# Kernel tuning notes

Hardware: AMD Instinct MI355X
Metric: run time of the kernel (lower is better)

Reference implementation:

```python
import jax, jax.numpy as jnp
import numpy as np

NEG_INF = -1e30


def setup_inputs() -> dict:
    key = jax.random.key(0)
    kq, kk, kv, ks = jax.random.split(key, 4)
    B, H, S, D = 2, 16, 2048, 64
    return {
        "q": jax.random.normal(kq, (B, H, S, D), dtype=jnp.float32),
        "k": jax.random.normal(kk, (B, H, S, D), dtype=jnp.float32),
        "v": jax.random.normal(kv, (B, H, S, D), dtype=jnp.float32),
        "sink_weights": jax.random.normal(ks, (H,), dtype=jnp.float32),
        "sliding_window": 1024,
    }


def reference(q, k, v, sink_weights, sliding_window):
    """Sliding-window causal attention with a learnable attention-sink logit.

    Equivalent to FlexAttention.forward with sink_weights given: an extra kv
    position (the sink) is appended whose score is replaced by sink_weights[h]
    and whose value is zero -> it only adds mass to the softmax denominator.
    """
    B, H, S_q, D = q.shape
    S_kv = k.shape[2]
    scale = 1.0 / np.sqrt(D)

    # [B, H, S_q, S_kv] raw scores
    scores = jnp.einsum("bhqd,bhkd->bhqk", q, k) * scale

    q_idx = jnp.arange(S_q)[:, None]
    kv_idx = jnp.arange(S_kv)[None, :]
    keep = (kv_idx <= q_idx) & (q_idx - kv_idx <= sliding_window)  # [S_q, S_kv]
    scores = jnp.where(keep[None, None], scores, NEG_INF)

    # sink column: per-head learnable logit, always visible
    sink_col = jnp.broadcast_to(
        sink_weights[None, :, None, None], (B, H, S_q, 1)
    )
    logits = jnp.concatenate([scores, sink_col], axis=-1)  # [B,H,S_q,S_kv+1]

    probs = jax.nn.softmax(logits, axis=-1)
    # sink value is zero, so only the first S_kv prob columns hit v
    out = jnp.einsum("bhqk,bhkd->bhqd", probs[..., :S_kv], v)
    return out
```

## Files before the change

kernel.cpp:

```cpp
#include <hip/hip_runtime.h>


typedef __bf16 bf16x8 __attribute__((ext_vector_type(8)));
typedef __bf16 bf16x4 __attribute__((ext_vector_type(4)));
typedef float  f32x16 __attribute__((ext_vector_type(16)));

#define NT 256
#define NEG_BIG (-3.0e38f)

__device__ __forceinline__ int swz(int row, int gran) {
    return row * 64 + ((gran ^ ((row >> 1) & 7)) << 3);
}

__device__ __forceinline__ bf16x4 xswap32(bf16x4 v) {
    union { bf16x4 v; int i[2]; } u;
    u.v = v;
    u.i[0] = __shfl_xor(u.i[0], 32, 64);
    u.i[1] = __shfl_xor(u.i[1], 32, 64);
    return u.v;
}

__device__ const int SEG_N[24] = {3,2,2,2,2,1,2,1, 1,1,1,1,1,1,1,1, 1,1,1,1,1,1,1,1};
__device__ const int SEG_IT[24][3] = {
  {0,1,2},{2,3,0},{3,4,0},{4,5,0},{5,6,0},{6,0,0},{6,7,0},{7,0,0},
  {8,0,0},{8,0,0},{9,0,0},{9,0,0},{10,0,0},{10,0,0},{11,0,0},{11,0,0},
  {12,0,0},{12,0,0},{13,0,0},{13,0,0},{14,0,0},{14,0,0},{15,0,0},{15,0,0}};
__device__ const int SEG_J0[24][3] = {
  {0,0,0},{3,0,0},{6,0,0},{7,0,0},{6,0,0},{3,0,0},{12,0,0},{7,0,0},
  {0,0,0},{9,0,0},{0,0,0},{9,0,0},{0,0,0},{9,0,0},{0,0,0},{9,0,0},
  {0,0,0},{9,0,0},{0,0,0},{9,0,0},{0,0,0},{9,0,0},{0,0,0},{9,0,0}};
__device__ const int SEG_J1[24][3] = {
  {2,4,3},{6,6,0},{8,7,0},{10,6,0},{12,3,0},{12,0,0},{14,7,0},{16,0,0},
  {9,0,0},{18,0,0},{9,0,0},{18,0,0},{9,0,0},{18,0,0},{9,0,0},{18,0,0},
  {9,0,0},{18,0,0},{9,0,0},{18,0,0},{9,0,0},{18,0,0},{9,0,0},{18,0,0}};
__device__ const int SEG_SX[24][3] = {
  {0,0,0},{1,0,0},{1,0,0},{1,0,0},{1,0,0},{1,0,0},{2,0,0},{1,0,0},
  {0,0,0},{1,0,0},{0,0,0},{1,0,0},{0,0,0},{1,0,0},{0,0,0},{1,0,0},
  {0,0,0},{1,0,0},{0,0,0},{1,0,0},{0,0,0},{1,0,0},{0,0,0},{1,0,0}};
__device__ const int NSEG_ITEM[16] = {1,1,2,2,2,2,3,2, 2,2,2,2,2,2,2,2};

__global__ __launch_bounds__(NT, 3) void flex_r9_main(
    const float* __restrict__ Q, const float* __restrict__ K,
    const float* __restrict__ V, const float* __restrict__ SINKW,
    const int* __restrict__ SWIN, void* __restrict__ WS,
    float* __restrict__ OUT, const int H, const int S)
{
    const int t    = threadIdx.x;
    const int lane = t & 63;
    const int w    = t >> 6;
    const int c    = lane & 31;
    const int hl   = lane >> 5;
    const int W    = SWIN[0];
    const float scale = 0.125f;

    const int NBH = gridDim.x / 24;
    const int bh  = blockIdx.x / 24;
    const int b24 = blockIdx.x - bh * 24;
    const int h   = bh % H;
    const float sw = SINKW[h];

    __shared__ __align__(16) __bf16 k_lds[2][64 * 64];
    __shared__ __align__(16) __bf16 v_lds[2][64 * 64];

    const size_t basebh = (size_t)bh * S * 64;
    const float4* kp4 = (const float4*)(K + basebh);
    const float4* vp4 = (const float4*)(V + basebh);
    __bf16* O_ws  = (__bf16*)WS;
    float2* ml_ws = (float2*)((char*)WS + (size_t)NBH * 48 * 16384);

    const int dgi = t & 15;
    const int kgi = t >> 4;
    float4 kreg[4], vreg[4];

    const int ns = SEG_N[b24];

    {
        const int it0 = SEG_IT[b24][0];
        const int ktA0 = (2 * it0 - 16 > 0) ? (2 * it0 - 16) : 0;
        const int kt = ktA0 + SEG_J0[b24][0];
        #pragma unroll
        for (int i = 0; i < 4; ++i) kreg[i] = kp4[kt * 1024 + i * NT + t];
        #pragma unroll
        for (int kk = 0; kk < 4; ++kk) vreg[kk] = vp4[kt * 1024 + (4 * kgi + kk) * 16 + dgi];
        #pragma unroll
        for (int i = 0; i < 4; ++i) {
            const int flat = i * NT + t;
            const int key = flat >> 4, dd = flat & 15;
            float4 f = kreg[i];
            bf16x4 b = { (__bf16)f.x, (__bf16)f.y, (__bf16)f.z, (__bf16)f.w };
            *(bf16x4*)&k_lds[0][swz(key, dd >> 1) + (dd & 1) * 4] = b;
        }
        {
            float4 a0 = vreg[0], a1 = vreg[1], a2 = vreg[2], a3 = vreg[3];
            bf16x4 w0 = { (__bf16)a0.x, (__bf16)a1.x, (__bf16)a2.x, (__bf16)a3.x };
            bf16x4 w1 = { (__bf16)a0.y, (__bf16)a1.y, (__bf16)a2.y, (__bf16)a3.y };
            bf16x4 w2 = { (__bf16)a0.z, (__bf16)a1.z, (__bf16)a2.z, (__bf16)a3.z };
            bf16x4 w3 = { (__bf16)a0.w, (__bf16)a1.w, (__bf16)a2.w, (__bf16)a3.w };
            const int gv = kgi >> 1, ov = (kgi & 1) * 4;
            *(bf16x4*)&v_lds[0][swz(4 * dgi + 0, gv) + ov] = w0;
            *(bf16x4*)&v_lds[0][swz(4 * dgi + 1, gv) + ov] = w1;
            *(bf16x4*)&v_lds[0][swz(4 * dgi + 2, gv) + ov] = w2;
            *(bf16x4*)&v_lds[0][swz(4 * dgi + 3, gv) + ov] = w3;
        }
    }

    int par = 0;

    for (int s = 0; s < ns; ++s) {
        const int item = SEG_IT[b24][s];
        const int j0   = SEG_J0[b24][s];
        const int j1   = SEG_J1[b24][s];
        const int sidx = SEG_SX[b24][s];
        const int ktA  = (2 * item - 16 > 0) ? (2 * item - 16) : 0;
        const int qw0  = item * 128 + 32 * w;
        const int qi   = qw0 + c;

        bf16x8 bq[4];
        {
            const float4* qp4 = (const float4*)(Q + basebh + (size_t)qi * 64);
            #pragma unroll
            for (int ks = 0; ks < 4; ++ks) {
                float4 f0 = qp4[4 * ks + 2 * hl];
                float4 f1 = qp4[4 * ks + 2 * hl + 1];
                bq[ks][0] = (__bf16)(f0.x * scale); bq[ks][1] = (__bf16)(f0.y * scale);
                bq[ks][2] = (__bf16)(f0.z * scale); bq[ks][3] = (__bf16)(f0.w * scale);
                bq[ks][4] = (__bf16)(f1.x * scale); bq[ks][5] = (__bf16)(f1.y * scale);
                bq[ks][6] = (__bf16)(f1.z * scale); bq[ks][7] = (__bf16)(f1.w * scale);
            }
        }

        float mrun = (sidx == 0) ? sw : NEG_BIG;
        float lrun = (sidx == 0) ? 1.0f : 0.0f;
        f32x16 accO0, accO1;
        #pragma unroll
        for (int i = 0; i < 16; ++i) { accO0[i] = 0.0f; accO1[i] = 0.0f; }

        for (int j = j0; j < j1; ++j) {
            const int k0 = (ktA + j) * 64;

            __syncthreads();

            int nkt = -1;
            if (j + 1 < j1) nkt = ktA + j + 1;
            else if (s + 1 < ns) {
                const int it2 = SEG_IT[b24][s + 1];
                const int ktA2 = (2 * it2 - 16 > 0) ? (2 * it2 - 16) : 0;
                nkt = ktA2 + SEG_J0[b24][s + 1];
            }
            if (nkt >= 0) {
                #pragma unroll
                for (int i = 0; i < 4; ++i) kreg[i] = kp4[nkt * 1024 + i * NT + t];
                #pragma unroll
                for (int kk = 0; kk < 4; ++kk) vreg[kk] = vp4[nkt * 1024 + (4 * kgi + kk) * 16 + dgi];
            }

            const __bf16* kb = k_lds[par];
            const __bf16* vb = v_lds[par];
            f32x16 accS0, accS1;
            #pragma unroll
            for (int i = 0; i < 16; ++i) { accS0[i] = 0.0f; accS1[i] = 0.0f; }
            #pragma unroll
            for (int ks = 0; ks < 4; ++ks) {
                bf16x8 ka0 = *(const bf16x8*)&kb[swz(c,      2 * ks + hl)];
                bf16x8 ka1 = *(const bf16x8*)&kb[swz(32 + c, 2 * ks + hl)];
                accS0 = __builtin_amdgcn_mfma_f32_32x32x16_bf16(ka0, bq[ks], accS0, 0, 0, 0);
                accS1 = __builtin_amdgcn_mfma_f32_32x32x16_bf16(ka1, bq[ks], accS1, 0, 0, 0);
            }

            const bool interior = (k0 + 63 <= qw0) && (qw0 + 31 - k0 <= W);
            if (!interior) {
                #pragma unroll
                for (int rg = 0; rg < 16; ++rg) {
                    const int kb2 = (rg & 3) + 8 * (rg >> 2) + 4 * hl;
                    const int ki0 = k0 + kb2, ki1 = k0 + 32 + kb2;
                    if (!((ki0 <= qi) && (qi - ki0 <= W))) accS0[rg] = -1e30f;
                    if (!((ki1 <= qi) && (qi - ki1 <= W))) accS1[rg] = -1e30f;
                }
            }

            float mx = accS0[0];
            #pragma unroll
            for (int i = 1; i < 16; ++i) mx = fmaxf(mx, accS0[i]);
            #pragma unroll
            for (int i = 0; i < 16; ++i) mx = fmaxf(mx, accS1[i]);
            mx = fmaxf(mx, __shfl_xor(mx, 32, 64));
            const float mnew  = fmaxf(mrun, mx);
            const float alpha = __expf(mrun - mnew);
            float ps = 0.0f;
            #pragma unroll
            for (int i = 0; i < 16; ++i) { float p = __expf(accS0[i] - mnew); accS0[i] = p; ps += p; }
            #pragma unroll
            for (int i = 0; i < 16; ++i) { float p = __expf(accS1[i] - mnew); accS1[i] = p; ps += p; }
            ps += __shfl_xor(ps, 32, 64);
            lrun = lrun * alpha + ps;
            mrun = mnew;
            #pragma unroll
            for (int i = 0; i < 16; ++i) { accO0[i] *= alpha; accO1[i] *= alpha; }

            bf16x4 qA = { (__bf16)accS0[0],  (__bf16)accS0[1],  (__bf16)accS0[2],  (__bf16)accS0[3]  };
            bf16x4 qB = { (__bf16)accS0[4],  (__bf16)accS0[5],  (__bf16)accS0[6],  (__bf16)accS0[7]  };
            bf16x4 qC = { (__bf16)accS0[8],  (__bf16)accS0[9],  (__bf16)accS0[10], (__bf16)accS0[11] };
            bf16x4 qD = { (__bf16)accS0[12], (__bf16)accS0[13], (__bf16)accS0[14], (__bf16)accS0[15] };
            bf16x4 qE = { (__bf16)accS1[0],  (__bf16)accS1[1],  (__bf16)accS1[2],  (__bf16)accS1[3]  };
            bf16x4 qF = { (__bf16)accS1[4],  (__bf16)accS1[5],  (__bf16)accS1[6],  (__bf16)accS1[7]  };
            bf16x4 qG = { (__bf16)accS1[8],  (__bf16)accS1[9],  (__bf16)accS1[10], (__bf16)accS1[11] };
            bf16x4 qH = { (__bf16)accS1[12], (__bf16)accS1[13], (__bf16)accS1[14], (__bf16)accS1[15] };
            bf16x4 r0 = xswap32(hl ? qA : qB);
            bf16x4 r1 = xswap32(hl ? qC : qD);
            bf16x4 r2 = xswap32(hl ? qE : qF);
            bf16x4 r3 = xswap32(hl ? qG : qH);
            bf16x4 lo0 = hl ? r0 : qA, hi0 = hl ? qB : r0;
            bf16x4 lo1 = hl ? r1 : qC, hi1 = hl ? qD : r1;
            bf16x4 lo2 = hl ? r2 : qE, hi2 = hl ? qF : r2;
            bf16x4 lo3 = hl ? r3 : qG, hi3 = hl ? qH : r3;
            bf16x8 bp[4];
            #pragma unroll
            for (int e = 0; e < 4; ++e) {
                bp[0][e] = lo0[e]; bp[0][4+e] = hi0[e];
                bp[1][e] = lo1[e]; bp[1][4+e] = hi1[e];
                bp[2][e] = lo2[e]; bp[2][4+e] = hi2[e];
                bp[3][e] = lo3[e]; bp[3][4+e] = hi3[e];
            }

            #pragma unroll
            for (int ks = 0; ks < 4; ++ks) {
                bf16x8 va0 = *(const bf16x8*)&vb[swz(c,      2 * ks + hl)];
                bf16x8 va1 = *(const bf16x8*)&vb[swz(32 + c, 2 * ks + hl)];
                accO0 = __builtin_amdgcn_mfma_f32_32x32x16_bf16(va0, bp[ks], accO0, 0, 0, 0);
                accO1 = __builtin_amdgcn_mfma_f32_32x32x16_bf16(va1, bp[ks], accO1, 0, 0, 0);
            }

            if (nkt >= 0) {
                const int np = par ^ 1;
                #pragma unroll
                for (int i = 0; i < 4; ++i) {
                    const int flat = i * NT + t;
                    const int key = flat >> 4, dd = flat & 15;
                    float4 f = kreg[i];
                    bf16x4 b = { (__bf16)f.x, (__bf16)f.y, (__bf16)f.z, (__bf16)f.w };
                    *(bf16x4*)&k_lds[np][swz(key, dd >> 1) + (dd & 1) * 4] = b;
                }
                float4 a0 = vreg[0], a1 = vreg[1], a2 = vreg[2], a3 = vreg[3];
                bf16x4 w0 = { (__bf16)a0.x, (__bf16)a1.x, (__bf16)a2.x, (__bf16)a3.x };
                bf16x4 w1 = { (__bf16)a0.y, (__bf16)a1.y, (__bf16)a2.y, (__bf16)a3.y };
                bf16x4 w2 = { (__bf16)a0.z, (__bf16)a1.z, (__bf16)a2.z, (__bf16)a3.z };
                bf16x4 w3 = { (__bf16)a0.w, (__bf16)a1.w, (__bf16)a2.w, (__bf16)a3.w };
                const int gv = kgi >> 1, ov = (kgi & 1) * 4;
                *(bf16x4*)&v_lds[np][swz(4 * dgi + 0, gv) + ov] = w0;
                *(bf16x4*)&v_lds[np][swz(4 * dgi + 1, gv) + ov] = w1;
                *(bf16x4*)&v_lds[np][swz(4 * dgi + 2, gv) + ov] = w2;
                *(bf16x4*)&v_lds[np][swz(4 * dgi + 3, gv) + ov] = w3;
            }
            par ^= 1;
        }

        if (item < 2) {
            const float inv = 1.0f / lrun;
            float* ob = OUT + basebh + (size_t)qi * 64;
            #pragma unroll
            for (int rg = 0; rg < 4; ++rg) {
                float4 f0 = { accO0[4*rg+0]*inv, accO0[4*rg+1]*inv,
                              accO0[4*rg+2]*inv, accO0[4*rg+3]*inv };
                float4 f1 = { accO1[4*rg+0]*inv, accO1[4*rg+1]*inv,
                              accO1[4*rg+2]*inv, accO1[4*rg+3]*inv };
                *(float4*)&ob[     8 * rg + 4 * hl] = f0;
                *(float4*)&ob[32 + 8 * rg + 4 * hl] = f1;
            }
        } else {
            const int slot = (bh * 16 + item) * 3 + sidx;
            const int qrel = 32 * w + c;
            if (hl == 0) ml_ws[(size_t)slot * 128 + qrel] = make_float2(mrun, lrun);
            __bf16* Os = O_ws + (size_t)slot * 8192 + (size_t)qrel * 64;
            #pragma unroll
            for (int qd = 0; qd < 4; ++qd) {
                const int d0 = 8 * qd + 4 * hl;
                bf16x4 b0 = { (__bf16)accO0[4*qd+0], (__bf16)accO0[4*qd+1],
                              (__bf16)accO0[4*qd+2], (__bf16)accO0[4*qd+3] };
                bf16x4 b1 = { (__bf16)accO1[4*qd+0], (__bf16)accO1[4*qd+1],
                              (__bf16)accO1[4*qd+2], (__bf16)accO1[4*qd+3] };
                *(bf16x4*)&Os[d0]      = b0;
                *(bf16x4*)&Os[32 + d0] = b1;
            }
        }
    }
}

__global__ __launch_bounds__(256) void flex_r9_combine(
    const void* __restrict__ WS, float* __restrict__ OUT, const int H, const int S)
{
    const int NBH  = gridDim.x / 14;
    const int bi   = blockIdx.x;
    const int bh   = bi / 14;
    const int item = 2 + (bi - bh * 14);
    const int ns   = NSEG_ITEM[item];
    const int t    = threadIdx.x;
    const int q    = t >> 1;
    const int half = t & 1;

    const __bf16* O_ws = (const __bf16*)WS;
    const float2* ml_ws = (const float2*)((const char*)WS + (size_t)NBH * 48 * 16384);
    const int base = (bh * 16 + item) * 3;

    float m[3], lv[3], a[3];
    float mst = NEG_BIG;
    for (int s = 0; s < ns; ++s) {
        float2 e = ml_ws[(size_t)(base + s) * 128 + q];
        m[s] = e.x; lv[s] = e.y;
        mst = fmaxf(mst, m[s]);
    }
    float lst = 0.0f;
    for (int s = 0; s < ns; ++s) { a[s] = __expf(m[s] - mst); lst += a[s] * lv[s]; }
    const float inv = 1.0f / lst;

    float acc[32];
    #pragma unroll
    for (int i = 0; i < 32; ++i) acc[i] = 0.0f;
    for (int s = 0; s < ns; ++s) {
        const __bf16* Os = O_ws + (size_t)(base + s) * 8192 + (size_t)q * 64 + 32 * half;
        const float as = a[s];
        #pragma unroll
        for (int v8 = 0; v8 < 4; ++v8) {
            bf16x8 o = *(const bf16x8*)&Os[8 * v8];
            #pragma unroll
            for (int jj = 0; jj < 8; ++jj) acc[8 * v8 + jj] += as * (float)o[jj];
        }
    }

    float* dst = OUT + (size_t)bh * S * 64 + (size_t)(item * 128 + q) * 64 + 32 * half;
    #pragma unroll
    for (int v4 = 0; v4 < 8; ++v4) {
        float4 f = { acc[4*v4+0] * inv, acc[4*v4+1] * inv,
                     acc[4*v4+2] * inv, acc[4*v4+3] * inv };
        *(float4*)&dst[4 * v4] = f;
    }
}

extern "C" void kernel_launch(void* const* d_in, const int* in_sizes, int n_in,
                              void* d_out, int out_size, void* d_ws, size_t ws_size,
                              hipStream_t stream) {
    const float* q     = (const float*)d_in[0];
    const float* k     = (const float*)d_in[1];
    const float* v     = (const float*)d_in[2];
    const float* sinkw = (const float*)d_in[3];
    const int*   swin  = (const int*)d_in[4];
    float* out = (float*)d_out;

    const int H = in_sizes[3];
    const int S = 2048;
    const int B = in_sizes[0] / (H * S * 64);
    const int NBH = B * H;

    flex_r9_main<<<dim3(NBH * 24), NT, 0, stream>>>(q, k, v, sinkw, swin, d_ws, out, H, S);
    flex_r9_combine<<<dim3(NBH * 14), 256, 0, stream>>>(d_ws, out, H, S);
}
```

Baseline: 138.7 us.

## Pre-convert K/V to swizzled bf16 image and stream it via global_load_lds

Adds a prep kernel that converts K and V to bf16 and writes them, pre-swizzled and with V transposed, into a scratch image stored in the output buffer. The main kernel then fills LDS directly with global_load_lds instead of loading fp32 into registers and converting in-loop, which cuts register pressure (launch bounds raised to 4 waves) and global traffic per tile. Work is rebalanced over 32 bins per head with up to 4 partial segments, and every query block now goes through the combine kernel. This adds an extra kernel launch, an extra full pass over K/V, and more workspace traffic for the combine step.

```diff
diff --git a/kernel.cpp b/kernel.cpp
--- a/kernel.cpp
+++ b/kernel.cpp
@@ -1,4 +1,5 @@
 #include <hip/hip_runtime.h>
+#include <cstdint>
 
 
 typedef __bf16 bf16x8 __attribute__((ext_vector_type(8)));
@@ -7,6 +8,13 @@
 
 #define NT 256
 #define NEG_BIG (-3.0e38f)
+
+typedef const __attribute__((address_space(1))) void gvoid;
+typedef __attribute__((address_space(3))) void lvoid;
+
+__device__ __forceinline__ void glds16(const void* g, void* l) {
+    __builtin_amdgcn_global_load_lds((gvoid*)g, (lvoid*)l, 16, 0, 0);
+}
 
 __device__ __forceinline__ int swz(int row, int gran) {
     return row * 64 + ((gran ^ ((row >> 1) & 7)) << 3);
@@ -20,30 +28,73 @@
     return u.v;
 }
 
-__device__ const int SEG_N[24] = {3,2,2,2,2,1,2,1, 1,1,1,1,1,1,1,1, 1,1,1,1,1,1,1,1};
-__device__ const int SEG_IT[24][3] = {
-  {0,1,2},{2,3,0},{3,4,0},{4,5,0},{5,6,0},{6,0,0},{6,7,0},{7,0,0},
-  {8,0,0},{8,0,0},{9,0,0},{9,0,0},{10,0,0},{10,0,0},{11,0,0},{11,0,0},
-  {12,0,0},{12,0,0},{13,0,0},{13,0,0},{14,0,0},{14,0,0},{15,0,0},{15,0,0}};
-__device__ const int SEG_J0[24][3] = {
-  {0,0,0},{3,0,0},{6,0,0},{7,0,0},{6,0,0},{3,0,0},{12,0,0},{7,0,0},
-  {0,0,0},{9,0,0},{0,0,0},{9,0,0},{0,0,0},{9,0,0},{0,0,0},{9,0,0},
-  {0,0,0},{9,0,0},{0,0,0},{9,0,0},{0,0,0},{9,0,0},{0,0,0},{9,0,0}};
-__device__ const int SEG_J1[24][3] = {
-  {2,4,3},{6,6,0},{8,7,0},{10,6,0},{12,3,0},{12,0,0},{14,7,0},{16,0,0},
-  {9,0,0},{18,0,0},{9,0,0},{18,0,0},{9,0,0},{18,0,0},{9,0,0},{18,0,0},
-  {9,0,0},{18,0,0},{9,0,0},{18,0,0},{9,0,0},{18,0,0},{9,0,0},{18,0,0}};
-__device__ const int SEG_SX[24][3] = {
-  {0,0,0},{1,0,0},{1,0,0},{1,0,0},{1,0,0},{1,0,0},{2,0,0},{1,0,0},
-  {0,0,0},{1,0,0},{0,0,0},{1,0,0},{0,0,0},{1,0,0},{0,0,0},{1,0,0},
-  {0,0,0},{1,0,0},{0,0,0},{1,0,0},{0,0,0},{1,0,0},{0,0,0},{1,0,0}};
-__device__ const int NSEG_ITEM[16] = {1,1,2,2,2,2,3,2, 2,2,2,2,2,2,2,2};
-
-__global__ __launch_bounds__(NT, 3) void flex_r9_main(
-    const float* __restrict__ Q, const float* __restrict__ K,
-    const float* __restrict__ V, const float* __restrict__ SINKW,
+__device__ const int SEG_N[32] = {
+  2,1,1,2,2,1,2,1, 2,1,2,1,1,2,1,1, 1,1,2,1,1,2,1,1, 1,1,2,1,1,2,1,1};
+__device__ const int SEG_IT[32][2] = {
+  {0,1},{2,0},{3,0},{3,4},{4,5},{5,0},{5,6},{6,0},
+  {6,7},{7,0},{7,8},{8,0},{8,0},{8,9},{9,0},{9,0},
+  {10,0},{10,0},{10,11},{11,0},{11,0},{11,12},{12,0},{12,0},
+  {13,0},{13,0},{13,14},{14,0},{14,0},{14,15},{15,0},{15,0}};
+__device__ const int SEG_J0[32][2] = {
+  {0,0},{0,0},{0,0},{7,0},{6,0},{3,0},{10,0},{5,0},
+  {12,0},{5,0},{12,0},{2,0},{9,0},{16,0},{5,0},{12,0},
+  {0,0},{7,0},{14,0},{3,0},{10,0},{17,0},{6,0},{12,0},
+  {0,0},{7,0},{14,0},{3,0},{10,0},{17,0},{6,0},{12,0}};
+__device__ const int SEG_J1[32][2] = {
+  {2,4},{6,0},{7,0},{8,6},{10,3},{10,0},{12,5},{12,0},
+  {14,5},{12,0},{16,2},{9,0},{16,0},{18,5},{12,0},{18,0},
+  {7,0},{14,0},{18,3},{10,0},{17,0},{18,6},{12,0},{18,0},
+  {7,0},{14,0},{18,3},{10,0},{17,0},{18,6},{12,0},{18,0}};
+__device__ const int SEG_SX[32][2] = {
+  {0,0},{0,0},{0,0},{1,0},{1,0},{1,0},{2,0},{1,0},
+  {2,0},{1,0},{2,0},{1,0},{2,0},{3,0},{1,0},{2,0},
+  {0,0},{1,0},{2,0},{1,0},{2,0},{3,0},{1,0},{2,0},
+  {0,0},{1,0},{2,0},{1,0},{2,0},{3,0},{1,0},{2,0}};
+__device__ const int NSEG16[16]      = {1,1,1,2,2,3,3,3,4,3,3,4,3,3,4,3};
+__device__ const int SLOT_BASE16[16] = {0,1,2,3,5,7,10,13,16,20,23,26,30,33,36,40};
+#define NSLOT 43
+
+__global__ __launch_bounds__(256) void flex_r11_prep(
+    const float* __restrict__ K, const float* __restrict__ V,
+    float* __restrict__ IMG, const int H, const int S)
+{
+    const int t  = threadIdx.x;
+    const int bh = blockIdx.x >> 5;
+    const int kt = blockIdx.x & 31;
+    const size_t basebh = (size_t)bh * S * 64;
+    const float4* kp4 = (const float4*)(K + basebh);
+    const float4* vp4 = (const float4*)(V + basebh);
+    __bf16* img = (__bf16*)IMG + ((size_t)bh * 32 + kt) * 8192;
+
+    #pragma unroll
+    for (int i = 0; i < 4; ++i) {
+        const int flat = i * 256 + t;
+        const int key = flat >> 4, dd = flat & 15;
+        float4 f = kp4[kt * 1024 + flat];
+        bf16x4 b = { (__bf16)f.x, (__bf16)f.y, (__bf16)f.z, (__bf16)f.w };
+        *(bf16x4*)&img[swz(key, dd >> 1) + (dd & 1) * 4] = b;
+    }
+    const int dgi = t & 15, kgi = t >> 4;
+    float4 a0 = vp4[kt * 1024 + (4 * kgi + 0) * 16 + dgi];
+    float4 a1 = vp4[kt * 1024 + (4 * kgi + 1) * 16 + dgi];
+    float4 a2 = vp4[kt * 1024 + (4 * kgi + 2) * 16 + dgi];
+    float4 a3 = vp4[kt * 1024 + (4 * kgi + 3) * 16 + dgi];
+    bf16x4 w0 = { (__bf16)a0.x, (__bf16)a1.x, (__bf16)a2.x, (__bf16)a3.x };
+    bf16x4 w1 = { (__bf16)a0.y, (__bf16)a1.y, (__bf16)a2.y, (__bf16)a3.y };
+    bf16x4 w2 = { (__bf16)a0.z, (__bf16)a1.z, (__bf16)a2.z, (__bf16)a3.z };
+    bf16x4 w3 = { (__bf16)a0.w, (__bf16)a1.w, (__bf16)a2.w, (__bf16)a3.w };
+    const int gv = kgi >> 1, ov = (kgi & 1) * 4;
+    __bf16* imgV = img + 4096;
+    *(bf16x4*)&imgV[swz(4 * dgi + 0, gv) + ov] = w0;
+    *(bf16x4*)&imgV[swz(4 * dgi + 1, gv) + ov] = w1;
+    *(bf16x4*)&imgV[swz(4 * dgi + 2, gv) + ov] = w2;
+    *(bf16x4*)&imgV[swz(4 * dgi + 3, gv) + ov] = w3;
+}
+
+__global__ __launch_bounds__(NT, 4) void flex_r11_main(
+    const float* __restrict__ Q, const float* __restrict__ SINKW,
     const int* __restrict__ SWIN, void* __restrict__ WS,
-    float* __restrict__ OUT, const int H, const int S)
+    const float* __restrict__ IMG, const int H, const int S)
 {
     const int t    = threadIdx.x;
     const int lane = t & 63;
@@ -53,9 +104,9 @@
     const int W    = SWIN[0];
     const float scale = 0.125f;
 
-    const int NBH = gridDim.x / 24;
-    const int bh  = blockIdx.x / 24;
-    const int b24 = blockIdx.x - bh * 24;
+    const int NBH = gridDim.x / 32;
+    const int bh  = blockIdx.x / 32;
+    const int bin = blockIdx.x - bh * 32;
     const int h   = bh % H;
     const float sw = SINKW[h];
 
@@ -63,54 +114,33 @@
     __shared__ __align__(16) __bf16 v_lds[2][64 * 64];
 
     const size_t basebh = (size_t)bh * S * 64;
-    const float4* kp4 = (const float4*)(K + basebh);
-    const float4* vp4 = (const float4*)(V + basebh);
+    const __bf16* kvimg = (const __bf16*)IMG + (size_t)bh * 32 * 8192;
     __bf16* O_ws  = (__bf16*)WS;
-    float2* ml_ws = (float2*)((char*)WS + (size_t)NBH * 48 * 16384);
-
-    const int dgi = t & 15;
-    const int kgi = t >> 4;
-    float4 kreg[4], vreg[4];
-
-    const int ns = SEG_N[b24];
+    float2* ml_ws = (float2*)((char*)WS + (size_t)NBH * NSLOT * 16384);
+
+    const int wb = (t >> 6) << 10;
+    const int ns = SEG_N[bin];
 
     {
-        const int it0 = SEG_IT[b24][0];
+        const int it0  = SEG_IT[bin][0];
         const int ktA0 = (2 * it0 - 16 > 0) ? (2 * it0 - 16) : 0;
-        const int kt = ktA0 + SEG_J0[b24][0];
-        #pragma unroll
-        for (int i = 0; i < 4; ++i) kreg[i] = kp4[kt * 1024 + i * NT + t];
-        #pragma unroll
-        for (int kk = 0; kk < 4; ++kk) vreg[kk] = vp4[kt * 1024 + (4 * kgi + kk) * 16 + dgi];
-        #pragma unroll
-        for (int i = 0; i < 4; ++i) {
-            const int flat = i * NT + t;
-            const int key = flat >> 4, dd = flat & 15;
-            float4 f = kreg[i];
-            bf16x4 b = { (__bf16)f.x, (__bf16)f.y, (__bf16)f.z, (__bf16)f.w };
-            *(bf16x4*)&k_lds[0][swz(key, dd >> 1) + (dd & 1) * 4] = b;
-        }
-        {
-            float4 a0 = vreg[0], a1 = vreg[1], a2 = vreg[2], a3 = vreg[3];
-            bf16x4 w0 = { (__bf16)a0.x, (__bf16)a1.x, (__bf16)a2.x, (__bf16)a3.x };
-            bf16x4 w1 = { (__bf16)a0.y, (__bf16)a1.y, (__bf16)a2.y, (__bf16)a3.y };
-            bf16x4 w2 = { (__bf16)a0.z, (__bf16)a1.z, (__bf16)a2.z, (__bf16)a3.z };
-            bf16x4 w3 = { (__bf16)a0.w, (__bf16)a1.w, (__bf16)a2.w, (__bf16)a3.w };
-            const int gv = kgi >> 1, ov = (kgi & 1) * 4;
-            *(bf16x4*)&v_lds[0][swz(4 * dgi + 0, gv) + ov] = w0;
-            *(bf16x4*)&v_lds[0][swz(4 * dgi + 1, gv) + ov] = w1;
-            *(bf16x4*)&v_lds[0][swz(4 * dgi + 2, gv) + ov] = w2;
-            *(bf16x4*)&v_lds[0][swz(4 * dgi + 3, gv) + ov] = w3;
-        }
+        const int kt   = ktA0 + SEG_J0[bin][0];
+        const char* g  = (const char*)(kvimg + (size_t)kt * 8192);
+        char* lk = (char*)&k_lds[0][0];
+        char* lv = (char*)&v_lds[0][0];
+        glds16(g +         t * 16, lk + wb);
+        glds16(g +  4096 + t * 16, lk + wb + 4096);
+        glds16(g +  8192 + t * 16, lv + wb);
+        glds16(g + 12288 + t * 16, lv + wb + 4096);
     }
 
     int par = 0;
 
     for (int s = 0; s < ns; ++s) {
-        const int item = SEG_IT[b24][s];
-        const int j0   = SEG_J0[b24][s];
-        const int j1   = SEG_J1[b24][s];
-        const int sidx = SEG_SX[b24][s];
+        const int item = SEG_IT[bin][s];
+        const int j0   = SEG_J0[bin][s];
+        const int j1   = SEG_J1[bin][s];
+        const int sidx = SEG_SX[bin][s];
         const int ktA  = (2 * item - 16 > 0) ? (2 * item - 16) : 0;
         const int qw0  = item * 128 + 32 * w;
         const int qi   = qw0 + c;
@@ -143,15 +173,19 @@
             int nkt = -1;
             if (j + 1 < j1) nkt = ktA + j + 1;
             else if (s + 1 < ns) {
-                const int it2 = SEG_IT[b24][s + 1];
+                const int it2  = SEG_IT[bin][s + 1];
                 const int ktA2 = (2 * it2 - 16 > 0) ? (2 * it2 - 16) : 0;
-                nkt = ktA2 + SEG_J0[b24][s + 1];
+                nkt = ktA2 + SEG_J0[bin][s + 1];
             }
             if (nkt >= 0) {
-                #pragma unroll
-                for (int i = 0; i < 4; ++i) kreg[i] = kp4[nkt * 1024 + i * NT + t];
-                #pragma unroll
-                for (int kk = 0; kk < 4; ++kk) vreg[kk] = vp4[nkt * 1024 + (4 * kgi + kk) * 16 + dgi];
+                const int np = par ^ 1;
+                const char* g = (const char*)(kvimg + (size_t)nkt * 8192);
+                char* lk = (char*)&k_lds[np][0];
+                char* lv = (char*)&v_lds[np][0];
+                glds16(g +         t * 16, lk + wb);
+                glds16(g +  4096 + t * 16, lk + wb + 4096);
+                glds16(g +  8192 + t * 16, lv + wb);
+                glds16(g + 12288 + t * 16, lv + wb + 4096);
             }
 
             const __bf16* kb = k_lds[par];
@@ -230,78 +264,43 @@
                 accO1 = __builtin_amdgcn_mfma_f32_32x32x16_bf16(va1, bp[ks], accO1, 0, 0, 0);
             }
 
-            if (nkt >= 0) {
-                const int np = par ^ 1;
-                #pragma unroll
-                for (int i = 0; i < 4; ++i) {
-                    const int flat = i * NT + t;
-                    const int key = flat >> 4, dd = flat & 15;
-                    float4 f = kreg[i];
-                    bf16x4 b = { (__bf16)f.x, (__bf16)f.y, (__bf16)f.z, (__bf16)f.w };
-                    *(bf16x4*)&k_lds[np][swz(key, dd >> 1) + (dd & 1) * 4] = b;
-                }
-                float4 a0 = vreg[0], a1 = vreg[1], a2 = vreg[2], a3 = vreg[3];
-                bf16x4 w0 = { (__bf16)a0.x, (__bf16)a1.x, (__bf16)a2.x, (__bf16)a3.x };
-                bf16x4 w1 = { (__bf16)a0.y, (__bf16)a1.y, (__bf16)a2.y, (__bf16)a3.y };
-                bf16x4 w2 = { (__bf16)a0.z, (__bf16)a1.z, (__bf16)a2.z, (__bf16)a3.z };
-                bf16x4 w3 = { (__bf16)a0.w, (__bf16)a1.w, (__bf16)a2.w, (__bf16)a3.w };
-                const int gv = kgi >> 1, ov = (kgi & 1) * 4;
-                *(bf16x4*)&v_lds[np][swz(4 * dgi + 0, gv) + ov] = w0;
-                *(bf16x4*)&v_lds[np][swz(4 * dgi + 1, gv) + ov] = w1;
-                *(bf16x4*)&v_lds[np][swz(4 * dgi + 2, gv) + ov] = w2;
-                *(bf16x4*)&v_lds[np][swz(4 * dgi + 3, gv) + ov] = w3;
-            }
             par ^= 1;
         }
 
-        if (item < 2) {
-            const float inv = 1.0f / lrun;
-            float* ob = OUT + basebh + (size_t)qi * 64;
-            #pragma unroll
-            for (int rg = 0; rg < 4; ++rg) {
-                float4 f0 = { accO0[4*rg+0]*inv, accO0[4*rg+1]*inv,
-                              accO0[4*rg+2]*inv, accO0[4*rg+3]*inv };
-                float4 f1 = { accO1[4*rg+0]*inv, accO1[4*rg+1]*inv,
-                              accO1[4*rg+2]*inv, accO1[4*rg+3]*inv };
-                *(float4*)&ob[     8 * rg + 4 * hl] = f0;
-                *(float4*)&ob[32 + 8 * rg + 4 * hl] = f1;
-            }
-        } else {
-            const int slot = (bh * 16 + item) * 3 + sidx;
-            const int qrel = 32 * w + c;
-            if (hl == 0) ml_ws[(size_t)slot * 128 + qrel] = make_float2(mrun, lrun);
-            __bf16* Os = O_ws + (size_t)slot * 8192 + (size_t)qrel * 64;
-            #pragma unroll
-            for (int qd = 0; qd < 4; ++qd) {
-                const int d0 = 8 * qd + 4 * hl;
-                bf16x4 b0 = { (__bf16)accO0[4*qd+0], (__bf16)accO0[4*qd+1],
-                              (__bf16)accO0[4*qd+2], (__bf16)accO0[4*qd+3] };
-                bf16x4 b1 = { (__bf16)accO1[4*qd+0], (__bf16)accO1[4*qd+1],
-                              (__bf16)accO1[4*qd+2], (__bf16)accO1[4*qd+3] };
-                *(bf16x4*)&Os[d0]      = b0;
-                *(bf16x4*)&Os[32 + d0] = b1;
-            }
+        const int slot = bh * NSLOT + SLOT_BASE16[item] + sidx;
+        const int qrel = 32 * w + c;
+        if (hl == 0) ml_ws[(size_t)slot * 128 + qrel] = make_float2(mrun, lrun);
+        __bf16* Os = O_ws + (size_t)slot * 8192 + (size_t)qrel * 64;
+        #pragma unroll
+        for (int qd = 0; qd < 4; ++qd) {
+            const int d0 = 8 * qd + 4 * hl;
+            bf16x4 b0 = { (__bf16)accO0[4*qd+0], (__bf16)accO0[4*qd+1],
+                          (__bf16)accO0[4*qd+2], (__bf16)accO0[4*qd+3] };
+            bf16x4 b1 = { (__bf16)accO1[4*qd+0], (__bf16)accO1[4*qd+1],
+                          (__bf16)accO1[4*qd+2], (__bf16)accO1[4*qd+3] };
+            *(bf16x4*)&Os[d0]      = b0;
+            *(bf16x4*)&Os[32 + d0] = b1;
         }
     }
 }
 
-__global__ __launch_bounds__(256) void flex_r9_combine(
+__global__ __launch_bounds__(256) void flex_r11_combine(
     const void* __restrict__ WS, float* __restrict__ OUT, const int H, const int S)
 {
-    const int NBH  = gridDim.x / 14;
+    const int NBH  = gridDim.x / 16;
     const int bi   = blockIdx.x;
-    const int bh   = bi / 14;
-    const int item = 2 + (bi - bh * 14);
-    const int ns   = NSEG_ITEM[item];
+    const int bh   = bi >> 4;
+    const int item = bi & 15;
+    const int ns   = NSEG16[item];
     const int t    = threadIdx.x;
     const int q    = t >> 1;
     const int half = t & 1;
 
-    const __bf16* O_ws = (const __bf16*)WS;
-    const float2* ml_ws = (const float2*)((const char*)WS + (size_t)NBH * 48 * 16384);
-    const int base = (bh * 16 + item) * 3;
-
-    float m[3], lv[3], a[3];
+    const __bf16* O_ws  = (const __bf16*)WS;
+    const float2* ml_ws = (const float2*)((const char*)WS + (size_t)NBH * NSLOT * 16384);
+    const int base = bh * NSLOT + SLOT_BASE16[item];
+
+    float m[4], lv[4], a[4];
     float mst = NEG_BIG;
     for (int s = 0; s < ns; ++s) {
         float2 e = ml_ws[(size_t)(base + s) * 128 + q];
@@ -350,6 +349,7 @@
     const int B = in_sizes[0] / (H * S * 64);
     const int NBH = B * H;
 
-    flex_r9_main<<<dim3(NBH * 24), NT, 0, stream>>>(q, k, v, sinkw, swin, d_ws, out, H, S);
-    flex_r9_combine<<<dim3(NBH * 14), 256, 0, stream>>>(d_ws, out, H, S);
-}
+    flex_r11_prep<<<dim3(NBH * 32), 256, 0, stream>>>(k, v, out, H, S);
+    flex_r11_main<<<dim3(NBH * 32), NT, 0, stream>>>(q, sinkw, swin, d_ws, out, H, S);
+    flex_r11_combine<<<dim3(NBH * 16), 256, 0, stream>>>(d_ws, out, H, S);
+}
```

Result: slower. 145.2 us (+4.6%).
